# Kernel optimization log

Measured on AMD Instinct MI355X. Metric: run time of the kernel, lower is better.

Reference implementation:

```python
import jax, jax.numpy as jnp
import numpy as np

DIM_MODEL = 1024
DIM_K = 1024
DIM_V = 1024


def setup_inputs() -> dict:
    key = jax.random.key(0)
    ks = jax.random.split(key, 7)
    B, S = 4, 2048
    scale = 1.0 / np.sqrt(DIM_MODEL)
    return {
        "x": jax.random.normal(ks[0], (B, S, DIM_MODEL), dtype=jnp.float32),
        # weights stored [in, out] (transpose of torch Linear.weight)
        "Wq": jax.random.normal(ks[1], (DIM_MODEL, DIM_K), dtype=jnp.float32) * scale,
        "Wk": jax.random.normal(ks[2], (DIM_MODEL, DIM_K), dtype=jnp.float32) * scale,
        "Wv": jax.random.normal(ks[3], (DIM_MODEL, DIM_V), dtype=jnp.float32) * scale,
        "Wo": jax.random.normal(ks[4], (DIM_V, DIM_MODEL), dtype=jnp.float32) * (1.0 / np.sqrt(DIM_V)),
        "ln2_gamma": jnp.ones((DIM_MODEL,), dtype=jnp.float32),
        "ln2_beta": jnp.zeros((DIM_MODEL,), dtype=jnp.float32),
    }


def _layernorm(x, gamma, beta, eps=1e-5):
    mu = jnp.mean(x, axis=-1, keepdims=True)
    var = jnp.var(x, axis=-1, keepdims=True)
    return (x - mu) * jax.lax.rsqrt(var + eps) * gamma + beta


def reference(x, Wq, Wk, Wv, Wo, ln2_gamma, ln2_beta):
    # single-head attention, x: [B,S,D]
    q = jnp.einsum("bsd,dk->bsk", x, Wq)
    k = jnp.einsum("bsd,dk->bsk", x, Wk)
    v = jnp.einsum("bsd,dv->bsv", x, Wv)
    scores = jnp.einsum("bqk,bsk->bqs", q, k) / jnp.sqrt(jnp.asarray(DIM_K, x.dtype))
    attn = jax.nn.softmax(scores, axis=-1)  # [B,S,S]
    ctx = jnp.einsum("bqs,bsv->bqv", attn, v)
    hidden = jnp.einsum("bqv,vd->bqd", ctx, Wo)
    hidden = _layernorm(hidden, ln2_gamma, ln2_beta)
    return hidden
```

## Files before the change

### kernel.cpp

```cpp
#include <hip/hip_runtime.h>
#include <hip/hip_bf16.h>
#include <stdint.h>

typedef __bf16 bf16;
typedef __attribute__((ext_vector_type(8))) __bf16 bf16x8;
typedef __attribute__((ext_vector_type(4))) __bf16 bf16x4;
typedef __attribute__((ext_vector_type(4))) float f32x4;

#define AS1 __attribute__((address_space(1)))
#define AS3 __attribute__((address_space(3)))

__device__ __forceinline__ void gl_lds16(const void* g, void* l) {
  __builtin_amdgcn_global_load_lds((const AS1 uint32_t*)g, (AS3 uint32_t*)l, 16, 0, 0);
}

#define FENCE() asm volatile("" ::: "memory")
#define BAR()                        \
  do {                               \
    FENCE();                         \
    __builtin_amdgcn_s_barrier();    \
    FENCE();                         \
  } while (0)
#define VMW4() asm volatile("s_waitcnt vmcnt(4)" ::: "memory")

template <int MODE>
__global__ __launch_bounds__(512, 2) void gemm256(
    const bf16* __restrict__ Abase, const bf16* __restrict__ Bbase,
    bf16* __restrict__ Cbase, int K, int lda, int ldb, int ldc,
    long long sA, long long sB, long long sC, float alpha,
    float* __restrict__ lsum, bf16* __restrict__ C2, bf16* __restrict__ C3) {
  extern __shared__ char smem[];
  const int z = blockIdx.z;
  const bf16* A = Abase + (long long)z * sA;
  const bf16* B = Bbase + (long long)z * sB;
  bf16* C = Cbase + (long long)z * sC;
  const int m0 = blockIdx.y * 256, n0 = blockIdx.x * 256;
  const int t = threadIdx.x;
  const int lane = t & 63;
  const int wid = t >> 6, wrow = wid >> 2, wcol = wid & 3;
  const int quad = lane >> 4, r = lane & 15;

  const int rowq = t >> 3;
  const int chunk = (t & 7) ^ (rowq & 7);
  const bf16* pA0 = A + (long long)(m0 + rowq) * lda + chunk * 8;
  const bf16* pB0 = B + (long long)(n0 + rowq) * ldb + chunk * 8;

  const int aoff = (wrow * 64 + r) * 128;
  const int boff = 32768 + (wcol * 32 + r) * 128;
  const int cs0 = ((quad) ^ (r & 7)) * 16;
  const int cs1 = ((4 + quad) ^ (r & 7)) * 16;

#define STAGE_A(HALF, KT, SB)                                                  \
  do {                                                                         \
    gl_lds16(pA0 + (long long)((HALF) * 128) * lda + (KT),                     \
             (SB) + (HALF) * 16384 + t * 16);                                  \
    gl_lds16(pA0 + (long long)((HALF) * 128 + 64) * lda + (KT),                \
             (SB) + (HALF) * 16384 + 8192 + t * 16);                           \
  } while (0)
#define STAGE_B(HALF, KT, SB)                                                  \
  do {                                                                         \
    gl_lds16(pB0 + (long long)((HALF) * 128) * ldb + (KT),                     \
             (SB) + 32768 + (HALF) * 16384 + t * 16);                          \
    gl_lds16(pB0 + (long long)((HALF) * 128 + 64) * ldb + (KT),                \
             (SB) + 32768 + (HALF) * 16384 + 8192 + t * 16);                   \
  } while (0)
#define READ_A(MH)                                                             \
  _Pragma("unroll") for (int mr = 0; mr < 4; ++mr) {                           \
    af[mr][0] = *(const bf16x8*)(Sc + (MH) * 16384 + aoff + mr * 2048 + cs0);  \
    af[mr][1] = *(const bf16x8*)(Sc + (MH) * 16384 + aoff + mr * 2048 + cs1);  \
  }
#define READ_B(NH)                                                             \
  _Pragma("unroll") for (int nr = 0; nr < 2; ++nr) {                           \
    bfr[NH][nr][0] =                                                           \
        *(const bf16x8*)(Sc + (NH) * 16384 + boff + nr * 2048 + cs0);          \
    bfr[NH][nr][1] =                                                           \
        *(const bf16x8*)(Sc + (NH) * 16384 + boff + nr * 2048 + cs1);          \
  }
#define MMA(MH, NH)                                                            \
  _Pragma("unroll") for (int mr = 0; mr < 4; ++mr)                             \
      _Pragma("unroll") for (int nr = 0; nr < 2; ++nr) {                       \
    acc[MH][NH][mr][nr] = __builtin_amdgcn_mfma_f32_16x16x32_bf16(             \
        af[mr][0], bfr[NH][nr][0], acc[MH][NH][mr][nr], 0, 0, 0);              \
    acc[MH][NH][mr][nr] = __builtin_amdgcn_mfma_f32_16x16x32_bf16(             \
        af[mr][1], bfr[NH][nr][1], acc[MH][NH][mr][nr], 0, 0, 0);              \
  }

  f32x4 acc[2][2][4][2] = {};
  bf16x8 af[4][2];
  bf16x8 bfr[2][2][2];
  char* Sc = smem;
  char* Sn = smem + 65536;
  const int T = K >> 6;

  STAGE_A(0, 0, Sc);
  STAGE_B(0, 0, Sc);
  STAGE_A(1, 0, Sc);
  STAGE_B(1, 0, Sc);
  {
    const int kt1p = (T > 1) ? 64 : 0;
    STAGE_A(0, kt1p, Sn);
    STAGE_B(0, kt1p, Sn);
  }
  VMW4();
  BAR();

  for (int tt = 0; tt < T; ++tt) {
    const int kt1 = (tt + 1 < T ? tt + 1 : 0) << 6;
    const int kt2 = (tt + 2 < T ? tt + 2 : 0) << 6;
    READ_A(0);
    READ_B(0);
    STAGE_A(1, kt1, Sn);
    __builtin_amdgcn_s_setprio(1);
    MMA(0, 0);
    __builtin_amdgcn_s_setprio(0);
    BAR();
    READ_B(1);
    STAGE_B(1, kt1, Sn);
    __builtin_amdgcn_s_setprio(1);
    MMA(0, 1);
    __builtin_amdgcn_s_setprio(0);
    BAR();
    READ_A(1);
    STAGE_A(0, kt2, Sc);
    __builtin_amdgcn_s_setprio(1);
    MMA(1, 0);
    __builtin_amdgcn_s_setprio(0);
    BAR();
    STAGE_B(0, kt2, Sc);
    __builtin_amdgcn_s_setprio(1);
    MMA(1, 1);
    __builtin_amdgcn_s_setprio(0);
    VMW4();
    BAR();
    char* tp = Sc;
    Sc = Sn;
    Sn = tp;
  }

#pragma unroll
  for (int mh = 0; mh < 2; ++mh)
#pragma unroll
    for (int mr = 0; mr < 4; ++mr) {
      const int row0 = m0 + mh * 128 + wrow * 64 + mr * 16 + quad * 4;
      float rsum[4] = {0.f, 0.f, 0.f, 0.f};
#pragma unroll
      for (int nh = 0; nh < 2; ++nh)
#pragma unroll
        for (int nr = 0; nr < 2; ++nr) {
          const int col = n0 + nh * 128 + wcol * 32 + nr * 16 + r;
#pragma unroll
          for (int rg = 0; rg < 4; ++rg) {
            float v = acc[mh][nh][mr][nr][rg] * alpha;
            if constexpr (MODE == 1) {
              bf16 eb = (bf16)__expf(v);
              C[(long long)(row0 + rg) * ldc + col] = eb;
              rsum[rg] += (float)eb;
            } else {
              C[(long long)(row0 + rg) * ldc + col] = (bf16)v;
            }
          }
        }
      if constexpr (MODE == 1) {
#pragma unroll
        for (int rg = 0; rg < 4; ++rg) {
#pragma unroll
          for (int off = 8; off >= 1; off >>= 1)
            rsum[rg] += __shfl_xor(rsum[rg], off);
          if (r == 0)
            atomicAdd(&lsum[(long long)z * 2048 + row0 + rg], rsum[rg]);
        }
      }
    }
#undef STAGE_A
#undef STAGE_B
#undef READ_A
#undef READ_B
#undef MMA
}

template <int MODE, bool SWZ>
__global__ __launch_bounds__(256, 3) void gemm128(
    const bf16* __restrict__ Abase, const bf16* __restrict__ Bbase,
    bf16* __restrict__ Cbase, int K, int lda, int ldb, int ldc,
    long long sA, long long sB, long long sC, float alpha,
    bf16* __restrict__ C2, bf16* __restrict__ C3) {
  extern __shared__ char smem[];
  int bx = blockIdx.x, by = blockIdx.y, bz = blockIdx.z;
  if constexpr (SWZ) {
    const int gx = gridDim.x, gy = gridDim.y;
    int id = bx + gx * (by + gy * bz);
    const int q = (gx * gy * (int)gridDim.z) >> 3;
    id = (id & 7) * q + (id >> 3);
    bx = id % gx;
    by = (id / gx) % gy;
    bz = id / (gx * gy);
  }
  const int z = bz;
  const bf16* A = Abase + (long long)z * sA;
  const bf16* B = Bbase + (long long)z * sB;
  bf16* C = Cbase + (long long)z * sC;
  const int m0 = by * 128, n0 = bx * 128;
  const int t = threadIdx.x;
  const int lane = t & 63, wave = t >> 6;
  const int wm = (wave >> 1) * 64, wn = (wave & 1) * 64;
  const int quad = lane >> 4, r = lane & 15;

  const int srow = t >> 3;
  const int schunk = (t & 7) ^ (srow & 7);
  const bf16* ga = A + (long long)(m0 + srow) * lda + schunk * 8;
  const bf16* gb = B + (long long)(n0 + srow) * ldb + schunk * 8;
  char* la = smem + t * 16;
  char* lb = smem + 16384 + t * 16;

  f32x4 acc[4][4] = {};

  for (int k0 = 0; k0 < K; k0 += 64) {
    __syncthreads();
#pragma unroll
    for (int rd = 0; rd < 4; rd++) {
      gl_lds16(ga + (long long)(32 * rd) * lda, la + rd * 4096);
      gl_lds16(gb + (long long)(32 * rd) * ldb, lb + rd * 4096);
    }
    ga += 64;
    gb += 64;
    __syncthreads();

#pragma unroll
    for (int kk = 0; kk < 2; kk++) {
      bf16x8 af[4], bfr[4];
      const int csa = ((kk * 4 + quad) ^ (r & 7)) * 16;
      const char* pa = smem + (wm + r) * 128 + csa;
      const char* pb = smem + 16384 + (wn + r) * 128 + csa;
#pragma unroll
      for (int i = 0; i < 4; i++) af[i] = *(const bf16x8*)(pa + i * 2048);
#pragma unroll
      for (int j = 0; j < 4; j++) bfr[j] = *(const bf16x8*)(pb + j * 2048);
#pragma unroll
      for (int i = 0; i < 4; i++)
#pragma unroll
        for (int j = 0; j < 4; j++)
          acc[i][j] = __builtin_amdgcn_mfma_f32_16x16x32_bf16(af[i], bfr[j],
                                                              acc[i][j], 0, 0, 0);
    }
  }

  if constexpr (MODE == 4) {
    bf16* dst;
    int c0;
    if (n0 < 1024) {
      dst = Cbase; c0 = n0;
    } else if (n0 < 2048) {
      dst = C2; c0 = n0 - 1024;
    } else {
      dst = C3; c0 = n0 - 2048;
    }
#pragma unroll
    for (int i = 0; i < 4; i++) {
      const int row0 = m0 + wm + i * 16 + quad * 4;
#pragma unroll
      for (int j = 0; j < 4; j++) {
        const int col = c0 + wn + j * 16 + r;
#pragma unroll
        for (int rg = 0; rg < 4; rg++)
          dst[(long long)(row0 + rg) * 1024 + col] = (bf16)acc[i][j][rg];
      }
    }
    return;
  }

#pragma unroll
  for (int i = 0; i < 4; i++) {
    const int row0 = m0 + wm + i * 16 + quad * 4;
#pragma unroll
    for (int j = 0; j < 4; j++) {
      const int col = n0 + wn + j * 16 + r;
#pragma unroll
      for (int rg = 0; rg < 4; rg++) {
        float v = acc[i][j][rg] * alpha;
        C[(long long)(row0 + rg) * ldc + col] = (bf16)v;
      }
    }
  }
}

__global__ __launch_bounds__(256) void prep(
    const float* __restrict__ x, const float* __restrict__ Wq,
    const float* __restrict__ Wk, const float* __restrict__ Wv,
    const float* __restrict__ Wo, bf16* __restrict__ Xb,
    bf16* __restrict__ Wcat, bf16* __restrict__ Wot,
    float* __restrict__ lsum) {
  __shared__ float tile[32][33];
  const int bx = blockIdx.x;
  const int t = threadIdx.x;
  if (bx < 4096) {
    if (bx < 32) lsum[bx * 256 + t] = 0.f;
    long long i = (long long)bx * 256 + t;
    const float4* p = (const float4*)x;
    float4 a = p[i * 2], b = p[i * 2 + 1];
    bf16x8 o;
    o[0] = (bf16)a.x; o[1] = (bf16)a.y; o[2] = (bf16)a.z; o[3] = (bf16)a.w;
    o[4] = (bf16)b.x; o[5] = (bf16)b.y; o[6] = (bf16)b.z; o[7] = (bf16)b.w;
    ((bf16x8*)Xb)[i] = o;
  } else {
    int idx = bx - 4096;
    const int zw = idx >> 10;
    idx &= 1023;
    const int tiy = idx >> 5, tix = idx & 31;
    const float* W = (zw == 0) ? Wq : (zw == 1) ? Wk : (zw == 2) ? Wv : Wo;
    bf16* dst = (zw < 3) ? (Wcat + (long long)zw * 1024 * 1024) : Wot;
    const int bx0 = tix * 32, by0 = tiy * 32;
    const int ttx = t & 31, tty = t >> 5;
#pragma unroll
    for (int i = 0; i < 32; i += 8)
      tile[tty + i][ttx] = W[(long long)(by0 + tty + i) * 1024 + bx0 + ttx];
    __syncthreads();
#pragma unroll
    for (int i = 0; i < 32; i += 8)
      dst[(long long)(bx0 + tty + i) * 1024 + by0 + ttx] = (bf16)tile[ttx][tty + i];
  }
}

__global__ __launch_bounds__(256) void layernorm_rows(
    const bf16* __restrict__ H, const float* __restrict__ lsum,
    const float* __restrict__ gamma, const float* __restrict__ beta,
    float* __restrict__ O) {
  const long long row = blockIdx.x;
  const bf16* h = H + row * 1024;
  float* o = O + row * 1024;
  const int t = threadIdx.x;
  const int lane = t & 63, wave = t >> 6;
  const float invl = 1.f / lsum[row];
  bf16x4 hv = ((const bf16x4*)h)[t];
  float v[4] = {(float)hv[0] * invl, (float)hv[1] * invl, (float)hv[2] * invl,
                (float)hv[3] * invl};
  float s = v[0] + v[1] + v[2] + v[3];
  float ss = v[0] * v[0] + v[1] * v[1] + v[2] * v[2] + v[3] * v[3];
#pragma unroll
  for (int off = 32; off >= 1; off >>= 1) {
    s += __shfl_xor(s, off);
    ss += __shfl_xor(ss, off);
  }
  __shared__ float rs[4], rss[4];
  if (lane == 0) {
    rs[wave] = s;
    rss[wave] = ss;
  }
  __syncthreads();
  s = rs[0] + rs[1] + rs[2] + rs[3];
  ss = rss[0] + rss[1] + rss[2] + rss[3];
  const float mean = s * (1.f / 1024.f);
  const float var = ss * (1.f / 1024.f) - mean * mean;
  const float rstd = rsqrtf(var + 1e-5f);
  float4 g = ((const float4*)gamma)[t];
  float4 bb = ((const float4*)beta)[t];
  float4 rr;
  rr.x = (v[0] - mean) * rstd * g.x + bb.x;
  rr.y = (v[1] - mean) * rstd * g.y + bb.y;
  rr.z = (v[2] - mean) * rstd * g.z + bb.z;
  rr.w = (v[3] - mean) * rstd * g.w + bb.w;
  ((float4*)o)[t] = rr;
}

extern "C" void kernel_launch(void* const* d_in, const int* in_sizes, int n_in,
                              void* d_out, int out_size, void* d_ws,
                              size_t ws_size, hipStream_t stream) {
  const float* x = (const float*)d_in[0];
  const float* Wq = (const float*)d_in[1];
  const float* Wk = (const float*)d_in[2];
  const float* Wv = (const float*)d_in[3];
  const float* Wo = (const float*)d_in[4];
  const float* gamma = (const float*)d_in[5];
  const float* beta = (const float*)d_in[6];
  float* out = (float*)d_out;

  const int LDP = 2112;

  char* ws = (char*)d_ws;
  const size_t MB = 1024ull * 1024ull;
  bf16* Xb = (bf16*)(ws + 0);
  bf16* Hd = (bf16*)(ws + 0);
  bf16* Wcat = (bf16*)(ws + 16 * MB);
  bf16* Wot = (bf16*)(ws + 22 * MB);
  bf16* Qd = (bf16*)(ws + 24 * MB);
  bf16* Kd = (bf16*)(ws + 40 * MB);
  bf16* Vd = (bf16*)(ws + 56 * MB);
  bf16* expS = (bf16*)(ws + 72 * MB);
  float* lsum = (float*)(ws + 105 * MB);
  bf16* VWo = (bf16*)(ws + 106 * MB);

  static int inited = 0;
  if (!inited) {
    hipFuncSetAttribute(reinterpret_cast<const void*>(&gemm256<1>),
                        hipFuncAttributeMaxDynamicSharedMemorySize, 131072);
    inited = 1;
  }

  prep<<<8192, 256, 0, stream>>>(x, Wq, Wk, Wv, Wo, Xb, Wcat, Wot, lsum);

  gemm128<4, false><<<dim3(24, 64, 1), 256, 32768, stream>>>(
      Xb, Wcat, Qd, 1024, 1024, 1024, 1024, 0, 0, 0, 1.f, Kd, Vd);

  gemm256<1><<<dim3(8, 8, 4), 512, 131072, stream>>>(
      Qd, Kd, expS, 1024, 1024, 1024, LDP, 2048 * 1024LL, 2048 * 1024LL,
      2048LL * LDP, 0.03125f, lsum, nullptr, nullptr);

  gemm128<0, false><<<dim3(16, 8, 4), 256, 32768, stream>>>(
      Wot, Vd, VWo, 1024, 1024, 1024, LDP, 0, 2048 * 1024LL, 1024LL * LDP,
      1.f, nullptr, nullptr);

  gemm128<0, true><<<dim3(8, 16, 4), 256, 32768, stream>>>(
      expS, VWo, Hd, 2048, LDP, LDP, 1024, 2048LL * LDP, 1024LL * LDP,
      2048 * 1024LL, 1.f, nullptr, nullptr);

  layernorm_rows<<<8192, 256, 0, stream>>>(Hd, lsum, gamma, beta, out);
}
```

Baseline: 274.2 us.

## Remove row padding and block swizzle, widen weight transpose tiles in prep

Drops the padded leading dimension (2112) for the score and VWo matrices in favour of unpadded 2048, and removes the block-index swizzle from the final context GEMM. It also moves Hd to its own workspace region, and rewrites the weight transpose in prep to use 64x64 tiles with float4 loads and bf16x4 stores. The padding and swizzle were meant to reduce cache/bank conflicts and improve L2 locality, so removing them risks channel conflicts from the power-of-two stride. The prep change aims at wider, more efficient memory accesses.

```diff
diff --git a/kernel.cpp b/kernel.cpp
--- a/kernel.cpp
+++ b/kernel.cpp
@@ -178,28 +178,18 @@
 #undef MMA
 }
 
-template <int MODE, bool SWZ>
+template <int MODE>
 __global__ __launch_bounds__(256, 3) void gemm128(
     const bf16* __restrict__ Abase, const bf16* __restrict__ Bbase,
     bf16* __restrict__ Cbase, int K, int lda, int ldb, int ldc,
     long long sA, long long sB, long long sC, float alpha,
     bf16* __restrict__ C2, bf16* __restrict__ C3) {
   extern __shared__ char smem[];
-  int bx = blockIdx.x, by = blockIdx.y, bz = blockIdx.z;
-  if constexpr (SWZ) {
-    const int gx = gridDim.x, gy = gridDim.y;
-    int id = bx + gx * (by + gy * bz);
-    const int q = (gx * gy * (int)gridDim.z) >> 3;
-    id = (id & 7) * q + (id >> 3);
-    bx = id % gx;
-    by = (id / gx) % gy;
-    bz = id / (gx * gy);
-  }
-  const int z = bz;
+  const int z = blockIdx.z;
   const bf16* A = Abase + (long long)z * sA;
   const bf16* B = Bbase + (long long)z * sB;
   bf16* C = Cbase + (long long)z * sC;
-  const int m0 = by * 128, n0 = bx * 128;
+  const int m0 = blockIdx.y * 128, n0 = blockIdx.x * 128;
   const int t = threadIdx.x;
   const int lane = t & 63, wave = t >> 6;
   const int wm = (wave >> 1) * 64, wn = (wave & 1) * 64;
@@ -289,7 +279,6 @@
     const float* __restrict__ Wo, bf16* __restrict__ Xb,
     bf16* __restrict__ Wcat, bf16* __restrict__ Wot,
     float* __restrict__ lsum) {
-  __shared__ float tile[32][33];
   const int bx = blockIdx.x;
   const int t = threadIdx.x;
   if (bx < 4096) {
@@ -302,21 +291,35 @@
     o[4] = (bf16)b.x; o[5] = (bf16)b.y; o[6] = (bf16)b.z; o[7] = (bf16)b.w;
     ((bf16x8*)Xb)[i] = o;
   } else {
+    __shared__ float tf[64][65];
     int idx = bx - 4096;
-    const int zw = idx >> 10;
-    idx &= 1023;
-    const int tiy = idx >> 5, tix = idx & 31;
+    const int zw = idx >> 8;
+    idx &= 255;
+    const int tiy = idx >> 4, tix = idx & 15;
     const float* W = (zw == 0) ? Wq : (zw == 1) ? Wk : (zw == 2) ? Wv : Wo;
     bf16* dst = (zw < 3) ? (Wcat + (long long)zw * 1024 * 1024) : Wot;
-    const int bx0 = tix * 32, by0 = tiy * 32;
-    const int ttx = t & 31, tty = t >> 5;
-#pragma unroll
-    for (int i = 0; i < 32; i += 8)
-      tile[tty + i][ttx] = W[(long long)(by0 + tty + i) * 1024 + bx0 + ttx];
+    const int r0 = tiy * 64, c0 = tix * 64;
+    const int rr = t >> 4, cc4 = (t & 15) * 4;
+#pragma unroll
+    for (int i = 0; i < 4; i++) {
+      float4 v =
+          *(const float4*)&W[(long long)(r0 + rr + 16 * i) * 1024 + c0 + cc4];
+      tf[rr + 16 * i][cc4] = v.x;
+      tf[rr + 16 * i][cc4 + 1] = v.y;
+      tf[rr + 16 * i][cc4 + 2] = v.z;
+      tf[rr + 16 * i][cc4 + 3] = v.w;
+    }
     __syncthreads();
 #pragma unroll
-    for (int i = 0; i < 32; i += 8)
-      dst[(long long)(bx0 + tty + i) * 1024 + by0 + ttx] = (bf16)tile[ttx][tty + i];
+    for (int i = 0; i < 4; i++) {
+      const int c = rr + 16 * i;
+      bf16x4 o;
+      o[0] = (bf16)tf[cc4][c];
+      o[1] = (bf16)tf[cc4 + 1][c];
+      o[2] = (bf16)tf[cc4 + 2][c];
+      o[3] = (bf16)tf[cc4 + 3][c];
+      *(bf16x4*)&dst[(long long)(c0 + c) * 1024 + r0 + cc4] = o;
+    }
   }
 }
 
@@ -373,20 +376,18 @@
   const float* beta = (const float*)d_in[6];
   float* out = (float*)d_out;
 
-  const int LDP = 2112;
-
   char* ws = (char*)d_ws;
   const size_t MB = 1024ull * 1024ull;
   bf16* Xb = (bf16*)(ws + 0);
-  bf16* Hd = (bf16*)(ws + 0);
   bf16* Wcat = (bf16*)(ws + 16 * MB);
   bf16* Wot = (bf16*)(ws + 22 * MB);
   bf16* Qd = (bf16*)(ws + 24 * MB);
   bf16* Kd = (bf16*)(ws + 40 * MB);
   bf16* Vd = (bf16*)(ws + 56 * MB);
   bf16* expS = (bf16*)(ws + 72 * MB);
-  float* lsum = (float*)(ws + 105 * MB);
-  bf16* VWo = (bf16*)(ws + 106 * MB);
+  float* lsum = (float*)(ws + 104 * MB);
+  bf16* VWo = (bf16*)(ws + 105 * MB);
+  bf16* Hd = (bf16*)(ws + 121 * MB);
 
   static int inited = 0;
   if (!inited) {
@@ -395,21 +396,21 @@
     inited = 1;
   }
 
-  prep<<<8192, 256, 0, stream>>>(x, Wq, Wk, Wv, Wo, Xb, Wcat, Wot, lsum);
-
-  gemm128<4, false><<<dim3(24, 64, 1), 256, 32768, stream>>>(
+  prep<<<5120, 256, 0, stream>>>(x, Wq, Wk, Wv, Wo, Xb, Wcat, Wot, lsum);
+
+  gemm128<4><<<dim3(24, 64, 1), 256, 32768, stream>>>(
       Xb, Wcat, Qd, 1024, 1024, 1024, 1024, 0, 0, 0, 1.f, Kd, Vd);
 
   gemm256<1><<<dim3(8, 8, 4), 512, 131072, stream>>>(
-      Qd, Kd, expS, 1024, 1024, 1024, LDP, 2048 * 1024LL, 2048 * 1024LL,
-      2048LL * LDP, 0.03125f, lsum, nullptr, nullptr);
-
-  gemm128<0, false><<<dim3(16, 8, 4), 256, 32768, stream>>>(
-      Wot, Vd, VWo, 1024, 1024, 1024, LDP, 0, 2048 * 1024LL, 1024LL * LDP,
+      Qd, Kd, expS, 1024, 1024, 1024, 2048, 2048 * 1024LL, 2048 * 1024LL,
+      2048 * 2048LL, 0.03125f, lsum, nullptr, nullptr);
+
+  gemm128<0><<<dim3(16, 8, 4), 256, 32768, stream>>>(
+      Wot, Vd, VWo, 1024, 1024, 1024, 2048, 0, 2048 * 1024LL, 1024 * 2048LL,
       1.f, nullptr, nullptr);
 
-  gemm128<0, true><<<dim3(8, 16, 4), 256, 32768, stream>>>(
-      expS, VWo, Hd, 2048, LDP, LDP, 1024, 2048LL * LDP, 1024LL * LDP,
+  gemm128<0><<<dim3(8, 16, 4), 256, 32768, stream>>>(
+      expS, VWo, Hd, 2048, 2048, 2048, 1024, 2048 * 2048LL, 1024 * 2048LL,
       2048 * 1024LL, 1.f, nullptr, nullptr);
 
   layernorm_rows<<<8192, 256, 0, stream>>>(Hd, lsum, gamma, beta, out);
```

After: 279.7 us. 2.0% more time.
